# Kernel optimization log

Measured on AMD Instinct MI355X. Metric: run time of the kernel, lower is better.

The kernel has to match this reference:

```python
import jax, jax.numpy as jnp
import numpy as np

KH, KW = 3, 3  # window_size[1], window_size[2]
FILTERS = 64
CHANNELS = 32
K = KH * KW * CHANNELS


def _extract_patches_valid(x, kh, kw):
    # TF tf.image.extract_patches ordering: (row_offset, col_offset, channel)
    B, H, W, C = x.shape
    Ho, Wo = H - kh + 1, W - kw + 1
    cols = [x[:, i:i + Ho, j:j + Wo, :] for i in range(kh) for j in range(kw)]
    return jnp.concatenate(cols, axis=-1)  # (B, Ho, Wo, kh*kw*C)


def setup_inputs() -> dict:
    key = jax.random.key(0)
    kx, kw = jax.random.split(key)
    x = jax.random.normal(kx, (8, 32, 32, CHANNELS), dtype=jnp.float32)
    # learned weight per __init__: shape (1, 1, 1, K, filters), random_normal init
    w = jax.random.normal(kw, (1, 1, 1, K, FILTERS), dtype=jnp.float32) * 0.05
    return {"x": x, "w": w}


def reference(x, w):
    # patches: (B, Ho, Wo, K)
    patches = _extract_patches_valid(x, KH, KW)
    # broadcast-add against weights: (B, Ho, Wo, K, filters)
    s = patches[..., None] + w[0, 0, 0]  # w[0,0,0]: (K, filters)
    # tropical conv: max over patch axis minus min over patch axis
    return jnp.max(s, axis=3) - jnp.min(s, axis=3)  # (B, Ho, Wo, filters)
```

## Files before the change

kernel.cpp:

```cpp
#include <hip/hip_runtime.h>


#define C_IN 32
#define NF 64
#define H_OUT 30
#define W_OUT 30
#define W_IN 32

typedef __attribute__((ext_vector_type(4))) float f32x4;

static __device__ __forceinline__ float max3f(float a, float b, float c) {
    return fmaxf(fmaxf(a, b), c);
}
static __device__ __forceinline__ float min3f(float a, float b, float c) {
    return fminf(fminf(a, b), c);
}

static __device__ __forceinline__ f32x4 sload16(const float* base, unsigned off_bytes) {
    f32x4 r;
    asm volatile("s_load_dwordx4 %0, %1, %2"
                 : "=s"(r)
                 : "s"(base), "s"(off_bytes));
    return r;
}

__global__ __launch_bounds__(512) void tropconv_kernel(
    const float* __restrict__ x,
    const float* __restrict__ w,
    float* __restrict__ out) {
    const int bx = blockIdx.x;
    const int q = bx & 3;
    const int bho = bx >> 2;
    const int b = bho / H_OUT;
    const int ho = bho - b * H_OUT;
    const int tid = threadIdx.x;
    const int lane = tid & 63;
    const int wave = __builtin_amdgcn_readfirstlane(tid >> 6);

    const int col0 = q * 8;
    const int npx = (q == 3) ? 6 : 8;

    __shared__ float pmx[8][8][NF];
    __shared__ float pmn[8][8][NF];

    const float* sbase = x + ((size_t)(b * 32 + ho) * W_IN) * C_IN + wave * 4;

    const int mcc = 31 - col0;
    unsigned coff[10];
    #pragma unroll
    for (int c = 0; c < 10; ++c) {
        const int cc = (c < mcc) ? c : mcc;
        coff[c] = (unsigned)((col0 + cc) * C_IN * 4);
    }

    const float* __restrict__ wbase = w + (size_t)(wave * 4) * NF + lane;

    float wc[4];
    #pragma unroll
    for (int cc = 0; cc < 4; ++cc) wc[cc] = wbase[cc * NF];

    f32x4 cur[8], nxt[8];
    #pragma unroll
    for (int px = 0; px < 8; ++px) cur[px] = sload16(sbase, coff[px]);

    float mx[8], mn[8];
    #pragma unroll
    for (int t = 0; t < 8; ++t) { mx[t] = -INFINITY; mn[t] = INFINITY; }

    #pragma unroll
    for (int ij = 0; ij < 9; ++ij) {
        asm volatile("s_waitcnt lgkmcnt(0)"
                     : "+s"(cur[0]), "+s"(cur[1]), "+s"(cur[2]), "+s"(cur[3]),
                       "+s"(cur[4]), "+s"(cur[5]), "+s"(cur[6]), "+s"(cur[7]));

        if (ij < 8) {
            const int i1 = (ij + 1) / 3;
            const int j1 = (ij + 1) - i1 * 3;
            const unsigned rowoff = (unsigned)(i1 * W_IN * C_IN * 4);
            #pragma unroll
            for (int px = 0; px < 8; ++px)
                nxt[px] = sload16(sbase, rowoff + coff[j1 + px]);
        }

        float wn[4];
        if (ij < 8) {
            #pragma unroll
            for (int cc = 0; cc < 4; ++cc)
                wn[cc] = wbase[((ij + 1) * C_IN + cc) * NF];
        }

        #pragma unroll
        for (int px = 0; px < 8; ++px) {
            const f32x4 p = cur[px];
            float s0 = p.x + wc[0];
            float s1 = p.y + wc[1];
            float s2 = p.z + wc[2];
            float s3 = p.w + wc[3];
            mx[px] = max3f(max3f(s0, s1, s2), s3, mx[px]);
            mn[px] = min3f(min3f(s0, s1, s2), s3, mn[px]);
        }

        if (ij < 8) {
            #pragma unroll
            for (int px = 0; px < 8; ++px) cur[px] = nxt[px];
            #pragma unroll
            for (int cc = 0; cc < 4; ++cc) wc[cc] = wn[cc];
        }
    }

    #pragma unroll
    for (int px = 0; px < 8; ++px) {
        pmx[wave][px][lane] = mx[px];
        pmn[wave][px][lane] = mn[px];
    }
    __syncthreads();

    const int nout = npx * NF;
    if (tid < nout) {
        const int px = tid >> 6;
        const int f = tid & 63;
        float a = fmaxf(fmaxf(fmaxf(pmx[0][px][f], pmx[1][px][f]),
                              fmaxf(pmx[2][px][f], pmx[3][px][f])),
                        fmaxf(fmaxf(pmx[4][px][f], pmx[5][px][f]),
                              fmaxf(pmx[6][px][f], pmx[7][px][f])));
        float m = fminf(fminf(fminf(pmn[0][px][f], pmn[1][px][f]),
                              fminf(pmn[2][px][f], pmn[3][px][f])),
                        fminf(fminf(pmn[4][px][f], pmn[5][px][f]),
                              fminf(pmn[6][px][f], pmn[7][px][f])));
        out[((size_t)bho * W_OUT + (col0 + px)) * NF + f] = a - m;
    }
}

extern "C" void kernel_launch(void* const* d_in, const int* in_sizes, int n_in,
                              void* d_out, int out_size, void* d_ws, size_t ws_size,
                              hipStream_t stream) {
    const float* x = (const float*)d_in[0];
    const float* w = (const float*)d_in[1];
    float* out = (float*)d_out;

    dim3 grid(8 * H_OUT * 4);
    dim3 block(512);
    tropconv_kernel<<<grid, block, 0, stream>>>(x, w, out);
}
```

Before: 64.93 us.

## Split channels across 16 waves and preload full 3x10 input window into SGPRs

New measurement: 68.79 us. 1.06x slower.

```diff
diff --git a/kernel.cpp b/kernel.cpp
--- a/kernel.cpp
+++ b/kernel.cpp
@@ -6,8 +6,9 @@
 #define H_OUT 30
 #define W_OUT 30
 #define W_IN 32
+#define NWAVE 16
 
-typedef __attribute__((ext_vector_type(4))) float f32x4;
+typedef __attribute__((ext_vector_type(2))) float f32x2;
 
 static __device__ __forceinline__ float max3f(float a, float b, float c) {
     return fmaxf(fmaxf(a, b), c);
@@ -16,15 +17,15 @@
     return fminf(fminf(a, b), c);
 }
 
-static __device__ __forceinline__ f32x4 sload16(const float* base, unsigned off_bytes) {
-    f32x4 r;
-    asm volatile("s_load_dwordx4 %0, %1, %2"
+static __device__ __forceinline__ f32x2 sload8(const float* base, unsigned off_bytes) {
+    f32x2 r;
+    asm volatile("s_load_dwordx2 %0, %1, %2"
                  : "=s"(r)
                  : "s"(base), "s"(off_bytes));
     return r;
 }
 
-__global__ __launch_bounds__(512) void tropconv_kernel(
+__global__ __launch_bounds__(1024) void tropconv_kernel(
     const float* __restrict__ x,
     const float* __restrict__ w,
     float* __restrict__ out) {
@@ -40,10 +41,8 @@
     const int col0 = q * 8;
     const int npx = (q == 3) ? 6 : 8;
 
-    __shared__ float pmx[8][8][NF];
-    __shared__ float pmn[8][8][NF];
-
-    const float* sbase = x + ((size_t)(b * 32 + ho) * W_IN) * C_IN + wave * 4;
+    __shared__ float pmx[NWAVE][8][NF];
+    __shared__ float pmn[NWAVE][8][NF];
 
     const int mcc = 31 - col0;
     unsigned coff[10];
@@ -53,58 +52,49 @@
         coff[c] = (unsigned)((col0 + cc) * C_IN * 4);
     }
 
-    const float* __restrict__ wbase = w + (size_t)(wave * 4) * NF + lane;
+    const float* rbase = x + (size_t)((b * 32 + ho) * W_IN) * C_IN + wave * 2;
 
-    float wc[4];
+    f32x2 rc[3][10];
     #pragma unroll
-    for (int cc = 0; cc < 4; ++cc) wc[cc] = wbase[cc * NF];
+    for (int r = 0; r < 3; ++r) {
+        const float* rb = rbase + (size_t)r * W_IN * C_IN;
+        #pragma unroll
+        for (int c = 0; c < 10; ++c) rc[r][c] = sload8(rb, coff[c]);
+    }
 
-    f32x4 cur[8], nxt[8];
+    const float* __restrict__ wbase = w + (size_t)(wave * 2) * NF + lane;
+    float w0[9], w1[9];
     #pragma unroll
-    for (int px = 0; px < 8; ++px) cur[px] = sload16(sbase, coff[px]);
+    for (int ij = 0; ij < 9; ++ij) {
+        w0[ij] = wbase[(ij * C_IN) * NF];
+        w1[ij] = wbase[(ij * C_IN + 1) * NF];
+    }
 
     float mx[8], mn[8];
     #pragma unroll
     for (int t = 0; t < 8; ++t) { mx[t] = -INFINITY; mn[t] = INFINITY; }
 
+    asm volatile("s_waitcnt lgkmcnt(0)");
+    #pragma unroll
+    for (int r = 0; r < 3; ++r) {
+        asm volatile(""
+                     : "+s"(rc[r][0]), "+s"(rc[r][1]), "+s"(rc[r][2]),
+                       "+s"(rc[r][3]), "+s"(rc[r][4]), "+s"(rc[r][5]),
+                       "+s"(rc[r][6]), "+s"(rc[r][7]), "+s"(rc[r][8]),
+                       "+s"(rc[r][9]));
+    }
+
     #pragma unroll
     for (int ij = 0; ij < 9; ++ij) {
-        asm volatile("s_waitcnt lgkmcnt(0)"
-                     : "+s"(cur[0]), "+s"(cur[1]), "+s"(cur[2]), "+s"(cur[3]),
-                       "+s"(cur[4]), "+s"(cur[5]), "+s"(cur[6]), "+s"(cur[7]));
-
-        if (ij < 8) {
-            const int i1 = (ij + 1) / 3;
-            const int j1 = (ij + 1) - i1 * 3;
-            const unsigned rowoff = (unsigned)(i1 * W_IN * C_IN * 4);
-            #pragma unroll
-            for (int px = 0; px < 8; ++px)
-                nxt[px] = sload16(sbase, rowoff + coff[j1 + px]);
-        }
-
-        float wn[4];
-        if (ij < 8) {
-            #pragma unroll
-            for (int cc = 0; cc < 4; ++cc)
-                wn[cc] = wbase[((ij + 1) * C_IN + cc) * NF];
-        }
-
+        const int i = ij / 3;
+        const int j = ij - i * 3;
         #pragma unroll
         for (int px = 0; px < 8; ++px) {
-            const f32x4 p = cur[px];
-            float s0 = p.x + wc[0];
-            float s1 = p.y + wc[1];
-            float s2 = p.z + wc[2];
-            float s3 = p.w + wc[3];
-            mx[px] = max3f(max3f(s0, s1, s2), s3, mx[px]);
-            mn[px] = min3f(min3f(s0, s1, s2), s3, mn[px]);
-        }
-
-        if (ij < 8) {
-            #pragma unroll
-            for (int px = 0; px < 8; ++px) cur[px] = nxt[px];
-            #pragma unroll
-            for (int cc = 0; cc < 4; ++cc) wc[cc] = wn[cc];
+            const f32x2 p = rc[i][j + px];
+            float s0 = p.x + w0[ij];
+            float s1 = p.y + w1[ij];
+            mx[px] = max3f(s0, s1, mx[px]);
+            mn[px] = min3f(s0, s1, mn[px]);
         }
     }
 
@@ -119,14 +109,13 @@
     if (tid < nout) {
         const int px = tid >> 6;
         const int f = tid & 63;
-        float a = fmaxf(fmaxf(fmaxf(pmx[0][px][f], pmx[1][px][f]),
-                              fmaxf(pmx[2][px][f], pmx[3][px][f])),
-                        fmaxf(fmaxf(pmx[4][px][f], pmx[5][px][f]),
-                              fmaxf(pmx[6][px][f], pmx[7][px][f])));
-        float m = fminf(fminf(fminf(pmn[0][px][f], pmn[1][px][f]),
-                              fminf(pmn[2][px][f], pmn[3][px][f])),
-                        fminf(fminf(pmn[4][px][f], pmn[5][px][f]),
-                              fminf(pmn[6][px][f], pmn[7][px][f])));
+        float a = pmx[0][px][f];
+        float m = pmn[0][px][f];
+        #pragma unroll
+        for (int ww = 1; ww < NWAVE; ++ww) {
+            a = fmaxf(a, pmx[ww][px][f]);
+            m = fminf(m, pmn[ww][px][f]);
+        }
         out[((size_t)bho * W_OUT + (col0 + px)) * NF + f] = a - m;
     }
 }
@@ -139,6 +128,6 @@
     float* out = (float*)d_out;
 
     dim3 grid(8 * H_OUT * 4);
-    dim3 block(512);
+    dim3 block(1024);
     tropconv_kernel<<<grid, block, 0, stream>>>(x, w, out);
 }
```
